# Performance work log

Measured on AMD Instinct MI355X. Metric: run time of the kernel, lower is better.

## Reference

```python
import jax, jax.numpy as jnp
import numpy as np
import math

D = 192            # base channel dim (init arg d); s has D channels
D2 = 2 * D         # y has 2d channels
H = 48; W = 48; BS = 2
NH = 8             # attention heads (divides both D2 and D)
NY = H * W         # tokens per image


def pe2d(d_model, height, width):
    """Faithful port of positionalencoding2d: (d_model, H, W)."""
    dh = d_model // 2
    div = jnp.exp(jnp.arange(0.0, dh, 2.0) * (-math.log(10000.0) / dh))  # (dh/2,)
    pw = jnp.arange(0.0, width)[:, None] * div    # (W, dh/2)
    ph = jnp.arange(0.0, height)[:, None] * div   # (H, dh/2)
    pe = jnp.zeros((d_model, height, width), jnp.float32)
    pe = pe.at[0:dh:2].set(jnp.broadcast_to(jnp.sin(pw).T[:, None, :], (dh // 2, height, width)))
    pe = pe.at[1:dh:2].set(jnp.broadcast_to(jnp.cos(pw).T[:, None, :], (dh // 2, height, width)))
    pe = pe.at[dh::2].set(jnp.broadcast_to(jnp.sin(ph).T[:, :, None], (dh // 2, height, width)))
    pe = pe.at[dh + 1::2].set(jnp.broadcast_to(jnp.cos(ph).T[:, :, None], (dh // 2, height, width)))
    return pe


def conv1x1(x, w, b):
    # x: (b,c,h,w), w: (out,c)
    return jnp.einsum('bchw,oc->bohw', x, w) + b[None, :, None, None]


def conv3x3(x, w, b):
    out = jax.lax.conv_general_dilated(x, w, (1, 1), 'SAME',
                                       dimension_numbers=('NCHW', 'OIHW', 'NCHW'))
    return out + b[None, :, None, None]


def bn(x, g, b):
    # inference-mode batchnorm with zero-mean / unit-var running stats
    return x * g[None, :, None, None] + b[None, :, None, None]


def setup_inputs() -> dict:
    key = jax.random.key(0)
    ks = jax.random.split(key, 8)
    r = lambda k, shp: jax.random.normal(k, shp, jnp.float32) * 0.02
    return {
        'y': jax.random.normal(ks[0], (BS, D2, H, W), jnp.float32),
        's': jax.random.normal(ks[1], (BS, D, H, W), jnp.float32),
        'wq_w': r(ks[2], (D2, D2)), 'wq_b': jnp.zeros((D2,), jnp.float32),
        'wk_w': r(ks[3], (D2, D2)), 'wk_b': jnp.zeros((D2,), jnp.float32),
        'wv_w': r(ks[4], (D, D)),   'wv_b': jnp.zeros((D,), jnp.float32),
        'conv1_w': r(ks[5], (D2, D2)), 'conv1_b': jnp.zeros((D2,), jnp.float32),
        'bn1_g': jnp.ones((D2,), jnp.float32), 'bn1_b': jnp.zeros((D2,), jnp.float32),
        'conv2_w': r(ks[6], (D, D)), 'conv2_b': jnp.zeros((D,), jnp.float32),
        'bn2_g': jnp.ones((D,), jnp.float32), 'bn2_b': jnp.zeros((D,), jnp.float32),
        'up_w': r(ks[7], (D2, D2, 3, 3)), 'up_b': jnp.zeros((D2,), jnp.float32),
        'conv3_w': r(jax.random.fold_in(key, 10), (D, D2)), 'conv3_b': jnp.zeros((D,), jnp.float32),
        'bn3_g': jnp.ones((D,), jnp.float32), 'bn3_b': jnp.zeros((D,), jnp.float32),
        'sig_w': r(jax.random.fold_in(key, 11), (D, D)), 'sig_b': jnp.zeros((D,), jnp.float32),
        'bnsig_g': jnp.ones((D,), jnp.float32), 'bnsig_b': jnp.zeros((D,), jnp.float32),
    }


def reference(y, s, wq_w, wq_b, wk_w, wk_b, wv_w, wv_b,
              conv1_w, conv1_b, bn1_g, bn1_b,
              conv2_w, conv2_b, bn2_g, bn2_b,
              up_w, up_b, conv3_w, conv3_b, bn3_g, bn3_b,
              sig_w, sig_b, bnsig_g, bnsig_b):
    bs = y.shape[0]
    y = y + pe2d(D2, H, W)[None]
    s = s + pe2d(D, H, W)[None]
    # conv+BN+ReLU feature extraction
    y_c1 = jax.nn.relu(bn(conv1x1(y, conv1_w, conv1_b), bn1_g, bn1_b))
    s_c2 = jax.nn.relu(bn(conv1x1(s, conv2_w, conv2_b), bn2_g, bn2_b))
    y_c3 = conv3x3(y, up_w, up_b)                                   # 'up' branch conv
    y_c3 = jax.nn.relu(bn(conv1x1(y_c3, conv3_w, conv3_b), bn3_g, bn3_b))  # (b, D, H, W)
    # tokenize
    yt = y_c1.reshape(bs, D2, NY).transpose(0, 2, 1)   # (b, ny, 2d)
    st = s_c2.reshape(bs, D, NY).transpose(0, 2, 1)    # (b, ny, d)
    # multi-head cross attention: Q,K from y-tokens, V from s-tokens
    Q = (yt @ wq_w.T + wq_b).reshape(bs, NY, NH, D2 // NH).transpose(0, 2, 1, 3)  # (b,h,ny,2d/h)
    K = (yt @ wk_w.T + wk_b).reshape(bs, NY, NH, D2 // NH).transpose(0, 2, 1, 3)
    V = (st @ wv_w.T + wv_b).reshape(bs, NY, NH, D // NH).transpose(0, 2, 1, 3)   # (b,h,ny,d/h)
    M = jnp.einsum('bhnd,bhmd->bhnm', Q, K) / math.sqrt(D)  # scale = d**0.5 as in source
    A = jax.nn.softmax(M, axis=-1)
    Z = jnp.einsum('bhnm,bhmd->bhnd', A, V)                 # (b,h,ny,d/h)
    Z = Z.transpose(0, 2, 1, 3).reshape(bs, NY, D).transpose(0, 2, 1).reshape(bs, D, H, W)
    # sigmoid gate and fuse
    g = jax.nn.sigmoid(bn(conv1x1(Z, sig_w, sig_b), bnsig_g, bnsig_b))
    Z = g * s
    return jnp.concatenate([Z, y_c3], axis=1)               # (b, 2d, H, W)
```

## Files before the change

kernel.cpp:

```cpp
#include <hip/hip_runtime.h>
#include <hip/hip_bf16.h>

#define Dc   192
#define D2c  384
#define NYc  2304

#define QSCALE 0.1041175462f

typedef __attribute__((ext_vector_type(8))) short short8;
typedef __attribute__((ext_vector_type(4))) float f32x4;

__device__ __forceinline__ unsigned short f2bf(float f) {
    unsigned int u = __float_as_uint(f);
    u += 0x7FFFu + ((u >> 16) & 1u);
    return (unsigned short)(u >> 16);
}
__device__ __forceinline__ float fexp2(float x) {
    float r; asm("v_exp_f32 %0, %1" : "=v"(r) : "v"(x)); return r;
}
__device__ __forceinline__ unsigned cvtpk(float lo, float hi) {
    unsigned r; asm("v_cvt_pk_bf16_f32 %0, %1, %2" : "=v"(r) : "v"(lo), "v"(hi));
    return r;
}
__device__ __forceinline__ int swz8(int bid, int nwg) {
    return (bid & 7) * (nwg >> 3) + (bid >> 3);
}

__global__ __launch_bounds__(256)
void build_pe_kernel(float* __restrict__ peY, float* __restrict__ peS) {
    int idx = blockIdx.x * 256 + threadIdx.x;
    int c, p, C; float* dst; int off;
    if (idx < 18432) { c = idx / 48; p = idx % 48; C = 384; dst = peY; off = idx; }
    else { int k = idx - 18432; c = k / 48; p = k % 48; C = 192; dst = peS; off = k; }
    int dh = C >> 1;
    int i = ((c < dh) ? c : c - dh) >> 1;
    float divv = expf((float)(2 * i) * (-9.210340371976184f / (float)dh));
    float ang = (float)p * divv;
    dst[off] = (c & 1) ? cosf(ang) : sinf(ang);
}

__global__ __launch_bounds__(256)
void prep_pe_kernel(const float* __restrict__ y, const float* __restrict__ s,
                    const float* __restrict__ peY, const float* __restrict__ peS,
                    unsigned short* __restrict__ ytok, unsigned short* __restrict__ stok,
                    float* __restrict__ sch) {
    __shared__ unsigned short T[64][66];
    int bid = blockIdx.x;
    int b, ct, nt, C; const float* in; const float* pe; unsigned short* outp; bool isS;
    if (bid < 432) { isS = false; b = bid / 216; int r = bid % 216; ct = r / 36; nt = r % 36;
                     in = y; pe = peY; outp = ytok; C = 384; }
    else { int l = bid - 432; isS = true; b = l / 108; int r = l % 108; ct = r / 36; nt = r % 36;
           in = s; pe = peS; outp = stok; C = 192; }
    int t = threadIdx.x;
    int nl = t & 63;
    int n = nt * 64 + nl;
    int pos_x = n % 48, pos_y = n / 48;
    #pragma unroll
    for (int i = 0; i < 16; ++i) {
        int cl = (t >> 6) + 4 * i;
        int c = ct * 64 + cl;
        int pos = (c < (C >> 1)) ? pos_x : pos_y;
        long gi = (long)b * C * NYc + (long)c * NYc + n;
        float v = in[gi] + pe[c * 48 + pos];
        if (isS) sch[gi] = v;
        T[nl][cl] = f2bf(v);
    }
    __syncthreads();
    #pragma unroll
    for (int i = 0; i < 8; ++i) {
        int nl2 = (t >> 5) + 8 * i;
        int cp  = t & 31;
        unsigned u = (unsigned)T[nl2][2 * cp] | ((unsigned)T[nl2][2 * cp + 1] << 16);
        long row = (long)b * NYc + nt * 64 + nl2;
        *(unsigned*)(outp + row * C + ct * 64 + 2 * cp) = u;
    }
}

__global__ __launch_bounds__(256)
void prep_w_kernel(const float* __restrict__ w0, const float* __restrict__ w1,
                   const float* __restrict__ w2, const float* __restrict__ w3,
                   const float* __restrict__ w4, const float* __restrict__ w5,
                   const float* __restrict__ w6, unsigned short* __restrict__ dst,
                   const float* __restrict__ wq_b, const float* __restrict__ wk_b,
                   float* __restrict__ qkb,
                   const float* __restrict__ upw, unsigned short* __restrict__ upwt) {
    int idx = blockIdx.x * 256 + threadIdx.x;
    if (idx < 626688) {
        if (idx < 768)
            qkb[idx] = (idx < 384) ? wq_b[idx] * QSCALE : wk_b[idx - 384];
        const float* src; int off; float scl = 1.0f;
        if      (idx < 147456) { src = w0; off = idx; }
        else if (idx < 294912) { src = w1; off = idx - 147456; scl = QSCALE; }
        else if (idx < 442368) { src = w2; off = idx - 294912; }
        else if (idx < 479232) { src = w3; off = idx - 442368; }
        else if (idx < 516096) { src = w4; off = idx - 479232; }
        else if (idx < 552960) { src = w5; off = idx - 516096; }
        else                   { src = w6; off = idx - 552960; }
        dst[idx] = f2bf(src[off] * scl);
    } else {
        int k = idx - 626688;
        int o = k / 3456; int r = k % 3456;
        int tap = r / 384;  int c = r % 384;
        upwt[k] = f2bf(upw[((long)o * 384 + c) * 9 + tap]);
    }
}

struct Seg {
    const unsigned short* A; const unsigned short* B;
    int aP, bP, K, nT, blkOff, nBlk, flags;
    const float *bias, *bng, *bnb;
    char* out; int oPitch; long oBatch;
};

template<int NSEG>
__global__ __launch_bounds__(256)
void fused_gemm(Seg s0, Seg s1, Seg s2, const float* __restrict__ smul)
{
    int raw = blockIdx.x;
    Seg sg = s0;
    if (NSEG > 1 && raw >= s1.blkOff) sg = s1;
    if (NSEG > 2 && raw >= s2.blkOff) sg = s2;
    int local = raw - sg.blkOff;
    local = (local & 7) * (sg.nBlk >> 3) + (local >> 3);
    int mt = local / sg.nT, nt = local - mt * sg.nT;
    int m0 = mt * 64, n0 = nt * 64;

    __shared__ __align__(16) unsigned short As[64][72];
    __shared__ __align__(16) unsigned short Bs[64][72];

    int t = threadIdx.x, lane = t & 63, w = t >> 6;
    int lr = lane & 15, lg = lane >> 4;
    int wm = (w >> 1) * 32, wn = (w & 1) * 32;

    f32x4 acc[2][2];
    #pragma unroll
    for (int i = 0; i < 2; ++i)
        #pragma unroll
        for (int j = 0; j < 2; ++j)
            acc[i][j] = (f32x4){0.f, 0.f, 0.f, 0.f};

    uint4 ra[2], rb[2];
    bool im2col = (sg.flags & 1) != 0;

    auto load = [&](int k0) {
        #pragma unroll
        for (int i = 0; i < 2; ++i) {
            int idx = t + i * 256, row = idx >> 3, sl = idx & 7;
            if (im2col) {
                int tok = m0 + row;
                int bb = tok >= NYc;
                int n = tok - bb * NYc;
                int tap = k0 / 384;
                int rem = k0 - tap * 384 + sl * 8;
                int py = n / 48 + tap / 3 - 1;
                int px = n % 48 + tap % 3 - 1;
                ra[i] = (py >= 0 && py < 48 && px >= 0 && px < 48)
                    ? *(const uint4*)(sg.A + ((long)bb * NYc + py * 48 + px) * sg.aP + rem)
                    : make_uint4(0, 0, 0, 0);
            } else {
                ra[i] = *(const uint4*)(sg.A + (long)(m0 + row) * sg.aP + k0 + sl * 8);
            }
            rb[i] = *(const uint4*)(sg.B + (long)(n0 + row) * sg.bP + k0 + sl * 8);
        }
    };
    auto store = [&]() {
        #pragma unroll
        for (int i = 0; i < 2; ++i) {
            int idx = t + i * 256;
            *(uint4*)&As[idx >> 3][(idx & 7) * 8] = ra[i];
            *(uint4*)&Bs[idx >> 3][(idx & 7) * 8] = rb[i];
        }
    };

    load(0); store(); __syncthreads();
    int NT = sg.K >> 6;
    for (int tt = 0; tt < NT; ++tt) {
        if (tt + 1 < NT) load((tt + 1) << 6);
        #pragma unroll
        for (int kk = 0; kk < 2; ++kk) {
            short8 a0 = *(const short8*)&As[wm + lr][kk * 32 + lg * 8];
            short8 a1 = *(const short8*)&As[wm + 16 + lr][kk * 32 + lg * 8];
            short8 b0 = *(const short8*)&Bs[wn + lr][kk * 32 + lg * 8];
            short8 b1 = *(const short8*)&Bs[wn + 16 + lr][kk * 32 + lg * 8];
            acc[0][0] = __builtin_amdgcn_mfma_f32_16x16x32_bf16(a0, b0, acc[0][0], 0, 0, 0);
            acc[0][1] = __builtin_amdgcn_mfma_f32_16x16x32_bf16(a0, b1, acc[0][1], 0, 0, 0);
            acc[1][0] = __builtin_amdgcn_mfma_f32_16x16x32_bf16(a1, b0, acc[1][0], 0, 0, 0);
            acc[1][1] = __builtin_amdgcn_mfma_f32_16x16x32_bf16(a1, b1, acc[1][1], 0, 0, 0);
        }
        __syncthreads();
        if (tt + 1 < NT) { store(); __syncthreads(); }
    }

    #pragma unroll
    for (int i = 0; i < 2; ++i)
    #pragma unroll
    for (int j = 0; j < 2; ++j)
    #pragma unroll
    for (int r = 0; r < 4; ++r) {
        int gm = m0 + wm + i * 16 + lg * 4 + r;
        int gn = n0 + wn + j * 16 + lr;
        int ch = (sg.flags & 8) ? gm : gn;
        float v = acc[i][j][r] + sg.bias[ch];
        if (sg.flags & 2)
            v = fmaxf(fmaf(v, sg.bng[ch], sg.bnb[ch]), 0.f);
        long o; int b = 0, tok = gn;
        if (sg.flags & 8) {
            b = gn >= NYc; tok = gn - b * NYc;
            o = (long)b * sg.oBatch + (long)gm * sg.oPitch + tok;
        } else {
            o = (long)gm * sg.oPitch + gn;
        }
        if (sg.flags & 16) {
            v = fmaf(v, sg.bng[ch], sg.bnb[ch]);
            v = 1.f / (1.f + __expf(-v));
            v *= smul[(long)b * 442368 + (long)gm * NYc + tok];
        }
        if (sg.flags & 4) ((float*)sg.out)[o] = v;
        else              ((unsigned short*)sg.out)[o] = f2bf(v);
    }
}

__global__ __launch_bounds__(512)
void attn_kernel(const unsigned short* __restrict__ QK,
                 const unsigned short* __restrict__ Vc,
                 unsigned short* __restrict__ Zt)
{
    int nid = swz8(blockIdx.x, 576);
    int qb = nid % 36;
    int bh = nid / 36;
    int b = bh >> 3, h = bh & 7;
    const unsigned short* Qg = QK + (long)b * NYc * 768 + h * 48;
    const unsigned short* Kg = Qg + 384;
    const unsigned short* Vg = Vc + ((long)b * Dc + h * 24) * NYc;
    unsigned short*       Z  = Zt + (long)b * NYc * Dc + h * 24;

    __shared__ __align__(16) unsigned short Ks_[128][72];
    __shared__ __align__(16) unsigned short Vs_[32][136];
    __shared__ __align__(16) unsigned int   Ps_[8][16][36];

    int t = threadIdx.x, lane = t & 63, w = t >> 6;
    int lr = lane & 15, lg = lane >> 4;
    int tm = w >> 1, hf = w & 1;
    int q0 = qb * 64;

    short8 z8 = {0, 0, 0, 0, 0, 0, 0, 0};
    const unsigned short* qrow = Qg + (long)(q0 + tm * 16 + lr) * 768;
    short8 bq0 = *(const short8*)(qrow + lg * 8);
    short8 bq1 = (lg < 2) ? *(const short8*)(qrow + 32 + lg * 8) : z8;

    float m_run = -1e30f, l_run = 0.f;
    f32x4 O0 = {0.f, 0.f, 0.f, 0.f}, O1 = {0.f, 0.f, 0.f, 0.f};

    for (int kt = 0; kt < 18; ++kt) {
        long k0 = kt * 128;
        #pragma unroll
        for (int i = 0; i < 2; ++i) {
            int idx = t + i * 512;
            int row = idx >> 3, sl = idx & 7;
            uint4 v = make_uint4(0, 0, 0, 0);
            if (sl < 6) v = *(const uint4*)(Kg + (k0 + row) * 768 + sl * 8);
            *(uint4*)&Ks_[row][sl * 8] = v;
        }
        if (t < 384) {
            int row = t >> 4, sl = t & 15;
            *(uint4*)&Vs_[row][sl * 8] =
                *(const uint4*)(Vg + (long)row * NYc + k0 + sl * 8);
        }
        __syncthreads();

        f32x4 sS[4];
        #pragma unroll
        for (int ks = 0; ks < 4; ++ks) {
            short8 ak0 = *(const short8*)&Ks_[hf * 64 + ks * 16 + lr][lg * 8];
            short8 ak1 = *(const short8*)&Ks_[hf * 64 + ks * 16 + lr][32 + lg * 8];
            f32x4 c = {0.f, 0.f, 0.f, 0.f};
            c = __builtin_amdgcn_mfma_f32_16x16x32_bf16(ak0, bq0, c, 0, 0, 0);
            c = __builtin_amdgcn_mfma_f32_16x16x32_bf16(ak1, bq1, c, 0, 0, 0);
            sS[ks] = c;
        }

        float tmax = -1e30f;
        #pragma unroll
        for (int ks = 0; ks < 4; ++ks)
            #pragma unroll
            for (int r = 0; r < 4; ++r) tmax = fmaxf(tmax, sS[ks][r]);
        tmax = fmaxf(tmax, __shfl_xor(tmax, 16));
        tmax = fmaxf(tmax, __shfl_xor(tmax, 32));

        if (__any(tmax > m_run + 10.f)) {
            float mn = fmaxf(m_run, tmax);
            float al = fexp2(m_run - mn);
            m_run = mn;
            l_run *= al;
            #pragma unroll
            for (int rr = 0; rr < 4; ++rr) {
                float arr = __shfl(al, (lane & 48) | (lg * 4 + rr));
                O0[rr] *= arr; O1[rr] *= arr;
            }
        }

        float psum = 0.f;
        #pragma unroll
        for (int ks = 0; ks < 4; ++ks) {
            float p0 = fexp2(sS[ks][0] - m_run);
            float p1 = fexp2(sS[ks][1] - m_run);
            float p2 = fexp2(sS[ks][2] - m_run);
            float p3 = fexp2(sS[ks][3] - m_run);
            psum += (p0 + p1) + (p2 + p3);
            Ps_[w][lr][8 * ks + 2 * lg]     = cvtpk(p0, p1);
            Ps_[w][lr][8 * ks + 2 * lg + 1] = cvtpk(p2, p3);
        }
        psum += __shfl_xor(psum, 16);
        psum += __shfl_xor(psum, 32);
        l_run += psum;

        short8 ap0 = *(const short8*)&Ps_[w][lr][4 * lg];
        short8 ap1 = *(const short8*)&Ps_[w][lr][16 + 4 * lg];
        short8 bv00 = *(const short8*)&Vs_[lr][hf * 64 + lg * 8];
        short8 bv01 = *(const short8*)&Vs_[lr][hf * 64 + 32 + lg * 8];
        short8 bv10 = *(const short8*)&Vs_[16 + lr][hf * 64 + lg * 8];
        short8 bv11 = *(const short8*)&Vs_[16 + lr][hf * 64 + 32 + lg * 8];
        O0 = __builtin_amdgcn_mfma_f32_16x16x32_bf16(ap0, bv00, O0, 0, 0, 0);
        O0 = __builtin_amdgcn_mfma_f32_16x16x32_bf16(ap1, bv01, O0, 0, 0, 0);
        O1 = __builtin_amdgcn_mfma_f32_16x16x32_bf16(ap0, bv10, O1, 0, 0, 0);
        O1 = __builtin_amdgcn_mfma_f32_16x16x32_bf16(ap1, bv11, O1, 0, 0, 0);
        __syncthreads();
    }

    float* Cf = (float*)&Ps_[0][0][0];
    float* T = Cf + tm * 576;
    if (hf == 1) {
        #pragma unroll
        for (int j = 0; j < 4; ++j) {
            T[lane * 8 + j]     = O0[j];
            T[lane * 8 + 4 + j] = O1[j];
        }
        if (lane < 16) { T[512 + lane] = m_run; T[528 + lane] = l_run; }
    }
    __syncthreads();
    if (hf == 0) {
        float mB = T[512 + lr], lB = T[528 + lr];
        float mS = fmaxf(m_run, mB);
        float aA = fexp2(m_run - mS), aB = fexp2(mB - mS);
        float invl = 1.f / (l_run * aA + lB * aB);
        float fA = aA * invl, fB = aB * invl;
        #pragma unroll
        for (int rr = 0; rr < 4; ++rr) {
            int src = (lane & 48) | (lg * 4 + rr);
            float gA = __shfl(fA, src), gB = __shfl(fB, src);
            int n = q0 + tm * 16 + lg * 4 + rr;
            unsigned short* zr = Z + (long)n * Dc;
            float z0 = O0[rr] * gA + T[lane * 8 + rr] * gB;
            zr[lr] = f2bf(z0);
            if (lr < 8) {
                float z1 = O1[rr] * gA + T[lane * 8 + 4 + rr] * gB;
                zr[16 + lr] = f2bf(z1);
            }
        }
    }
}

extern "C" void kernel_launch(void* const* d_in, const int* in_sizes, int n_in,
                              void* d_out, int out_size, void* d_ws, size_t ws_size,
                              hipStream_t stream) {
    const float* y       = (const float*)d_in[0];
    const float* s       = (const float*)d_in[1];
    const float* wq_w    = (const float*)d_in[2];
    const float* wq_b    = (const float*)d_in[3];
    const float* wk_w    = (const float*)d_in[4];
    const float* wk_b    = (const float*)d_in[5];
    const float* wv_w    = (const float*)d_in[6];
    const float* wv_b    = (const float*)d_in[7];
    const float* conv1_w = (const float*)d_in[8];
    const float* conv1_b = (const float*)d_in[9];
    const float* bn1_g   = (const float*)d_in[10];
    const float* bn1_b   = (const float*)d_in[11];
    const float* conv2_w = (const float*)d_in[12];
    const float* conv2_b = (const float*)d_in[13];
    const float* bn2_g   = (const float*)d_in[14];
    const float* bn2_b   = (const float*)d_in[15];
    const float* up_w    = (const float*)d_in[16];
    const float* up_b    = (const float*)d_in[17];
    const float* conv3_w = (const float*)d_in[18];
    const float* conv3_b = (const float*)d_in[19];
    const float* bn3_g   = (const float*)d_in[20];
    const float* bn3_b   = (const float*)d_in[21];
    const float* sig_w   = (const float*)d_in[22];
    const float* sig_b   = (const float*)d_in[23];
    const float* bnsig_g = (const float*)d_in[24];
    const float* bnsig_b = (const float*)d_in[25];

    unsigned short* wsp   = (unsigned short*)d_ws;
    unsigned short* wcvt  = wsp;
    unsigned short* upwt  = wcvt + 626688;
    unsigned short* y_pe  = upwt + 1327104;
    unsigned short* s_pe  = y_pe + 1769472;
    unsigned short* y_c1  = s_pe + 884736;
    unsigned short* s_c2  = y_c1 + 1769472;
    unsigned short* y_up  = s_c2 + 884736;
    unsigned short* QKtok = y_up + 1769472;
    unsigned short* Vch   = QKtok + 3538944;
    unsigned short* Ztok  = Vch + 884736;
    float*          s_ch  = (float*)(Ztok + 884736);
    float*          qkb   = s_ch + 884736;
    float*          peY   = qkb + 768;
    float*          peS   = peY + 18432;

    const unsigned short* conv1wb = wcvt;
    const unsigned short* wqkb    = wcvt + 147456;
    const unsigned short* conv2wb = wcvt + 442368;
    const unsigned short* wvb     = wcvt + 479232;
    const unsigned short* sigwb   = wcvt + 516096;
    const unsigned short* conv3wb = wcvt + 552960;

    build_pe_kernel<<<108, 256, 0, stream>>>(peY, peS);
    prep_w_kernel<<<7632, 256, 0, stream>>>(conv1_w, wq_w, wk_w, conv2_w,
                                            wv_w, sig_w, conv3_w, wcvt,
                                            wq_b, wk_b, qkb, up_w, upwt);
    prep_pe_kernel<<<648, 256, 0, stream>>>(y, s, peY, peS, y_pe, s_pe, s_ch);

    Seg sz = {};

    {
        Seg a = { y_pe, upwt, D2c, 9 * D2c, 9 * D2c, 6, 0, 432, 1,
                  up_b, nullptr, nullptr, (char*)y_up, D2c, 0 };
        Seg b = { y_pe, conv1wb, D2c, D2c, D2c, 6, 432, 432, 2,
                  conv1_b, bn1_g, bn1_b, (char*)y_c1, D2c, 0 };
        Seg c = { s_pe, conv2wb, Dc, Dc, Dc, 3, 864, 216, 2,
                  conv2_b, bn2_g, bn2_b, (char*)s_c2, Dc, 0 };
        fused_gemm<3><<<1080, 256, 0, stream>>>(a, b, c, nullptr);
    }
    {
        Seg a = { y_c1, wqkb, D2c, D2c, D2c, 12, 0, 864, 0,
                  qkb, nullptr, nullptr, (char*)QKtok, 768, 0 };
        Seg b = { conv3wb, y_up, D2c, D2c, D2c, 72, 864, 216, 2 | 4 | 8,
                  conv3_b, bn3_g, bn3_b,
                  (char*)((float*)d_out + (long)Dc * NYc), NYc, 884736 };
        Seg c = { wvb, s_c2, Dc, Dc, Dc, 72, 1080, 216, 8,
                  wv_b, nullptr, nullptr, (char*)Vch, NYc, 442368 };
        fused_gemm<3><<<1296, 256, 0, stream>>>(a, b, c, nullptr);
    }
    attn_kernel<<<576, 512, 0, stream>>>(QKtok, Vch, Ztok);
    {
        Seg a = { sigwb, Ztok, Dc, Dc, Dc, 72, 0, 216, 4 | 8 | 16,
                  sig_b, bnsig_g, bnsig_b, (char*)d_out, NYc, 884736 };
        fused_gemm<1><<<216, 256, 0, stream>>>(a, sz, sz, s_ch);
    }
}
```

Measured before the change: 198.5 us.

## Fold conv3 into up conv weights, split-K the fused conv, double-buffer GEMM

Since conv3 (1x1) follows the up 3x3 conv with no nonlinearity between them, the change precomposes the conv3 and up weights into one 192x3456 matrix and a combined bias. The fused 3x3-then-1x1 conv then runs as a single split-K (3-way) im2col GEMM whose bf16 partials are summed by a new reduce kernel that applies BN and ReLU. This removes the 384-channel y_up intermediate and the separate conv3 GEMM. The GEMM kernel also gains double-buffered LDS with one barrier per K step and a remainder-aware block swizzle. The risks are extra bf16 rounding of the partials and of the composed weights, plus an extra weight-composition GEMM and reduce launch.

```diff
diff --git a/kernel.cpp b/kernel.cpp
--- a/kernel.cpp
+++ b/kernel.cpp
@@ -15,6 +15,9 @@
     u += 0x7FFFu + ((u >> 16) & 1u);
     return (unsigned short)(u >> 16);
 }
+__device__ __forceinline__ float bf2f(unsigned short u) {
+    return __uint_as_float((unsigned)u << 16);
+}
 __device__ __forceinline__ float fexp2(float x) {
     float r; asm("v_exp_f32 %0, %1" : "=v"(r) : "v"(x)); return r;
 }
@@ -22,8 +25,10 @@
     unsigned r; asm("v_cvt_pk_bf16_f32 %0, %1, %2" : "=v"(r) : "v"(lo), "v"(hi));
     return r;
 }
-__device__ __forceinline__ int swz8(int bid, int nwg) {
-    return (bid & 7) * (nwg >> 3) + (bid >> 3);
+__device__ __forceinline__ int swzb(int orig, int nwg) {
+    int q = nwg >> 3, r = nwg & 7, x = orig & 7;
+    int base = (x < r) ? x * (q + 1) : r * (q + 1) + (x - r) * q;
+    return base + (orig >> 3);
 }
 
 __global__ __launch_bounds__(256)
@@ -83,7 +88,9 @@
                    const float* __restrict__ w6, unsigned short* __restrict__ dst,
                    const float* __restrict__ wq_b, const float* __restrict__ wk_b,
                    float* __restrict__ qkb,
-                   const float* __restrict__ upw, unsigned short* __restrict__ upwt) {
+                   const float* __restrict__ upw, unsigned short* __restrict__ upT,
+                   const float* __restrict__ up_b, const float* __restrict__ conv3_b,
+                   float* __restrict__ c3b) {
     int idx = blockIdx.x * 256 + threadIdx.x;
     if (idx < 626688) {
         if (idx < 768)
@@ -97,17 +104,23 @@
         else if (idx < 552960) { src = w5; off = idx - 516096; }
         else                   { src = w6; off = idx - 552960; }
         dst[idx] = f2bf(src[off] * scl);
-    } else {
+    } else if (idx < 1953792) {
         int k = idx - 626688;
-        int o = k / 3456; int r = k % 3456;
-        int tap = r / 384;  int c = r % 384;
-        upwt[k] = f2bf(upw[((long)o * 384 + c) * 9 + tap]);
+        int j = k / 384, m = k % 384;
+        int tap = j / 384, c = j % 384;
+        upT[k] = f2bf(upw[((long)m * 384 + c) * 9 + tap]);
+    } else if (idx < 1953984) {
+        int o = idx - 1953792;
+        float acc = 0.f;
+        for (int m = 0; m < 384; ++m) acc += w6[o * 384 + m] * up_b[m];
+        c3b[o] = acc + conv3_b[o];
     }
 }
 
 struct Seg {
     const unsigned short* A; const unsigned short* B;
-    int aP, bP, K, nT, blkOff, nBlk, flags;
+    int aP, bP, K, nT, blkOff, nBlk, flags, nSplit;
+    long oSplitBytes;
     const float *bias, *bng, *bnb;
     char* out; int oPitch; long oBatch;
 };
@@ -120,13 +133,20 @@
     Seg sg = s0;
     if (NSEG > 1 && raw >= s1.blkOff) sg = s1;
     if (NSEG > 2 && raw >= s2.blkOff) sg = s2;
-    int local = raw - sg.blkOff;
-    local = (local & 7) * (sg.nBlk >> 3) + (local >> 3);
+    int local = swzb(raw - sg.blkOff, sg.nBlk);
+    int kBase = 0;
+    if (sg.nSplit > 1) {
+        int pc = sg.nBlk / sg.nSplit;
+        int g = local / pc; local -= g * pc;
+        sg.A += (long)g * sg.K;
+        sg.out += (long)g * sg.oSplitBytes;
+        kBase = g * sg.K;
+    }
     int mt = local / sg.nT, nt = local - mt * sg.nT;
     int m0 = mt * 64, n0 = nt * 64;
 
-    __shared__ __align__(16) unsigned short As[64][72];
-    __shared__ __align__(16) unsigned short Bs[64][72];
+    __shared__ __align__(16) unsigned short As[2][64][72];
+    __shared__ __align__(16) unsigned short Bs[2][64][72];
 
     int t = threadIdx.x, lane = t & 63, w = t >> 6;
     int lr = lane & 15, lg = lane >> 4;
@@ -140,55 +160,59 @@
             acc[i][j] = (f32x4){0.f, 0.f, 0.f, 0.f};
 
     uint4 ra[2], rb[2];
-    bool im2col = (sg.flags & 1) != 0;
+    bool im2colB = (sg.flags & 1) != 0;
 
     auto load = [&](int k0) {
         #pragma unroll
         for (int i = 0; i < 2; ++i) {
             int idx = t + i * 256, row = idx >> 3, sl = idx & 7;
-            if (im2col) {
-                int tok = m0 + row;
+            ra[i] = *(const uint4*)(sg.A + (long)(m0 + row) * sg.aP + k0 + sl * 8);
+            if (im2colB) {
+                int tok = n0 + row;
                 int bb = tok >= NYc;
                 int n = tok - bb * NYc;
-                int tap = k0 / 384;
-                int rem = k0 - tap * 384 + sl * 8;
+                int kk = kBase + k0;
+                int tap = kk / 384;
+                int rem = kk - tap * 384 + sl * 8;
                 int py = n / 48 + tap / 3 - 1;
                 int px = n % 48 + tap % 3 - 1;
-                ra[i] = (py >= 0 && py < 48 && px >= 0 && px < 48)
-                    ? *(const uint4*)(sg.A + ((long)bb * NYc + py * 48 + px) * sg.aP + rem)
+                rb[i] = (py >= 0 && py < 48 && px >= 0 && px < 48)
+                    ? *(const uint4*)(sg.B + ((long)bb * NYc + py * 48 + px) * sg.bP + rem)
                     : make_uint4(0, 0, 0, 0);
             } else {
-                ra[i] = *(const uint4*)(sg.A + (long)(m0 + row) * sg.aP + k0 + sl * 8);
+                rb[i] = *(const uint4*)(sg.B + (long)(n0 + row) * sg.bP + k0 + sl * 8);
             }
-            rb[i] = *(const uint4*)(sg.B + (long)(n0 + row) * sg.bP + k0 + sl * 8);
         }
     };
-    auto store = [&]() {
+    auto store = [&](int buf) {
         #pragma unroll
         for (int i = 0; i < 2; ++i) {
             int idx = t + i * 256;
-            *(uint4*)&As[idx >> 3][(idx & 7) * 8] = ra[i];
-            *(uint4*)&Bs[idx >> 3][(idx & 7) * 8] = rb[i];
+            *(uint4*)&As[buf][idx >> 3][(idx & 7) * 8] = ra[i];
+            *(uint4*)&Bs[buf][idx >> 3][(idx & 7) * 8] = rb[i];
         }
     };
 
-    load(0); store(); __syncthreads();
+    load(0); store(0); __syncthreads();
     int NT = sg.K >> 6;
+    int cur = 0;
     for (int tt = 0; tt < NT; ++tt) {
-        if (tt + 1 < NT) load((tt + 1) << 6);
+        bool more = (tt + 1 < NT);
+        if (more) load((tt + 1) << 6);
         #pragma unroll
         for (int kk = 0; kk < 2; ++kk) {
-            short8 a0 = *(const short8*)&As[wm + lr][kk * 32 + lg * 8];
-            short8 a1 = *(const short8*)&As[wm + 16 + lr][kk * 32 + lg * 8];
-            short8 b0 = *(const short8*)&Bs[wn + lr][kk * 32 + lg * 8];
-            short8 b1 = *(const short8*)&Bs[wn + 16 + lr][kk * 32 + lg * 8];
+            short8 a0 = *(const short8*)&As[cur][wm + lr][kk * 32 + lg * 8];
+            short8 a1 = *(const short8*)&As[cur][wm + 16 + lr][kk * 32 + lg * 8];
+            short8 b0 = *(const short8*)&Bs[cur][wn + lr][kk * 32 + lg * 8];
+            short8 b1 = *(const short8*)&Bs[cur][wn + 16 + lr][kk * 32 + lg * 8];
             acc[0][0] = __builtin_amdgcn_mfma_f32_16x16x32_bf16(a0, b0, acc[0][0], 0, 0, 0);
             acc[0][1] = __builtin_amdgcn_mfma_f32_16x16x32_bf16(a0, b1, acc[0][1], 0, 0, 0);
             acc[1][0] = __builtin_amdgcn_mfma_f32_16x16x32_bf16(a1, b0, acc[1][0], 0, 0, 0);
             acc[1][1] = __builtin_amdgcn_mfma_f32_16x16x32_bf16(a1, b1, acc[1][1], 0, 0, 0);
         }
+        if (more) store(cur ^ 1);
         __syncthreads();
-        if (tt + 1 < NT) { store(); __syncthreads(); }
+        cur ^= 1;
     }
 
     #pragma unroll
@@ -200,7 +224,8 @@
         int gm = m0 + wm + i * 16 + lg * 4 + r;
         int gn = n0 + wn + j * 16 + lr;
         int ch = (sg.flags & 8) ? gm : gn;
-        float v = acc[i][j][r] + sg.bias[ch];
+        float v = acc[i][j][r];
+        if (!(sg.flags & 32)) v += sg.bias[ch];
         if (sg.flags & 2)
             v = fmaxf(fmaf(v, sg.bng[ch], sg.bnb[ch]), 0.f);
         long o; int b = 0, tok = gn;
@@ -220,12 +245,38 @@
     }
 }
 
+__global__ __launch_bounds__(256)
+void reduce_up_kernel(const unsigned short* __restrict__ part,
+                      const float* __restrict__ c3b,
+                      const float* __restrict__ bn3g, const float* __restrict__ bn3b,
+                      float* __restrict__ out) {
+    int tid = blockIdx.x * 256 + threadIdx.x;
+    int e = tid * 4;
+    int b = e / 442368; int r = e - b * 442368;
+    int o = r / 2304;
+    ushort4 p0 = *(const ushort4*)(part + e);
+    ushort4 p1 = *(const ushort4*)(part + 884736 + e);
+    ushort4 p2 = *(const ushort4*)(part + 1769472 + e);
+    float g = bn3g[o], bb = bn3b[o], cb = c3b[o];
+    float4 res;
+    float* rp = (float*)&res;
+    unsigned short* q0 = (unsigned short*)&p0;
+    unsigned short* q1 = (unsigned short*)&p1;
+    unsigned short* q2 = (unsigned short*)&p2;
+    #pragma unroll
+    for (int j = 0; j < 4; ++j) {
+        float v = bf2f(q0[j]) + bf2f(q1[j]) + bf2f(q2[j]) + cb;
+        rp[j] = fmaxf(fmaf(v, g, bb), 0.f);
+    }
+    *(float4*)(out + (long)b * 884736 + 442368 + r) = res;
+}
+
 __global__ __launch_bounds__(512)
 void attn_kernel(const unsigned short* __restrict__ QK,
                  const unsigned short* __restrict__ Vc,
                  unsigned short* __restrict__ Zt)
 {
-    int nid = swz8(blockIdx.x, 576);
+    int nid = swzb(blockIdx.x, 576);
     int qb = nid % 36;
     int bh = nid / 36;
     int b = bh >> 3, h = bh & 7;
@@ -392,18 +443,20 @@
 
     unsigned short* wsp   = (unsigned short*)d_ws;
     unsigned short* wcvt  = wsp;
-    unsigned short* upwt  = wcvt + 626688;
-    unsigned short* y_pe  = upwt + 1327104;
+    unsigned short* upT   = wcvt + 626688;
+    unsigned short* Wc    = upT + 1327104;
+    unsigned short* y_pe  = Wc + 663552;
     unsigned short* s_pe  = y_pe + 1769472;
     unsigned short* y_c1  = s_pe + 884736;
     unsigned short* s_c2  = y_c1 + 1769472;
-    unsigned short* y_up  = s_c2 + 884736;
-    unsigned short* QKtok = y_up + 1769472;
+    unsigned short* QKtok = s_c2 + 884736;
     unsigned short* Vch   = QKtok + 3538944;
-    unsigned short* Ztok  = Vch + 884736;
-    float*          s_ch  = (float*)(Ztok + 884736);
+    unsigned short* partZ = Vch + 884736;
+    unsigned short* Ztok  = partZ;
+    float*          s_ch  = (float*)(partZ + 2654208);
     float*          qkb   = s_ch + 884736;
-    float*          peY   = qkb + 768;
+    float*          c3b   = qkb + 768;
+    float*          peY   = c3b + 192;
     float*          peS   = peY + 18432;
 
     const unsigned short* conv1wb = wcvt;
@@ -414,35 +467,41 @@
     const unsigned short* conv3wb = wcvt + 552960;
 
     build_pe_kernel<<<108, 256, 0, stream>>>(peY, peS);
-    prep_w_kernel<<<7632, 256, 0, stream>>>(conv1_w, wq_w, wk_w, conv2_w,
+    prep_w_kernel<<<7633, 256, 0, stream>>>(conv1_w, wq_w, wk_w, conv2_w,
                                             wv_w, sig_w, conv3_w, wcvt,
-                                            wq_b, wk_b, qkb, up_w, upwt);
+                                            wq_b, wk_b, qkb, up_w, upT,
+                                            up_b, conv3_b, c3b);
     prep_pe_kernel<<<648, 256, 0, stream>>>(y, s, peY, peS, y_pe, s_pe, s_ch);
 
     Seg sz = {};
 
     {
-        Seg a = { y_pe, upwt, D2c, 9 * D2c, 9 * D2c, 6, 0, 432, 1,
-                  up_b, nullptr, nullptr, (char*)y_up, D2c, 0 };
-        Seg b = { y_pe, conv1wb, D2c, D2c, D2c, 6, 432, 432, 2,
-                  conv1_b, bn1_g, bn1_b, (char*)y_c1, D2c, 0 };
-        Seg c = { s_pe, conv2wb, Dc, Dc, Dc, 3, 864, 216, 2,
-                  conv2_b, bn2_g, bn2_b, (char*)s_c2, Dc, 0 };
-        fused_gemm<3><<<1080, 256, 0, stream>>>(a, b, c, nullptr);
+        Seg a = { conv3wb, upT, 384, 384, 384, 54, 0, 162, 32, 1, 0,
+                  nullptr, nullptr, nullptr, (char*)Wc, 3456, 0 };
+        fused_gemm<1><<<162, 256, 0, stream>>>(a, sz, sz, nullptr);
     }
     {
-        Seg a = { y_c1, wqkb, D2c, D2c, D2c, 12, 0, 864, 0,
+        Seg a = { Wc, y_pe, 3456, 384, 1152, 72, 0, 648, 1 | 8 | 32, 3,
+                  (long)884736 * 2,
+                  nullptr, nullptr, nullptr, (char*)partZ, NYc, 442368 };
+        Seg b = { y_pe, conv1wb, 384, 384, 384, 6, 648, 432, 2, 1, 0,
+                  conv1_b, bn1_g, bn1_b, (char*)y_c1, 384, 0 };
+        Seg c = { s_pe, conv2wb, 192, 192, 192, 3, 1080, 216, 2, 1, 0,
+                  conv2_b, bn2_g, bn2_b, (char*)s_c2, 192, 0 };
+        fused_gemm<3><<<1296, 256, 0, stream>>>(a, b, c, nullptr);
+    }
+    {
+        Seg a = { y_c1, wqkb, 384, 384, 384, 12, 0, 864, 0, 1, 0,
                   qkb, nullptr, nullptr, (char*)QKtok, 768, 0 };
-        Seg b = { conv3wb, y_up, D2c, D2c, D2c, 72, 864, 216, 2 | 4 | 8,
-                  conv3_b, bn3_g, bn3_b,
-                  (char*)((float*)d_out + (long)Dc * NYc), NYc, 884736 };
-        Seg c = { wvb, s_c2, Dc, Dc, Dc, 72, 1080, 216, 8,
+        Seg b = { wvb, s_c2, 192, 192, 192, 72, 864, 216, 8, 1, 0,
                   wv_b, nullptr, nullptr, (char*)Vch, NYc, 442368 };
-        fused_gemm<3><<<1296, 256, 0, stream>>>(a, b, c, nullptr);
-    }
+        fused_gemm<2><<<1080, 256, 0, stream>>>(a, b, sz, nullptr);
+    }
+    reduce_up_kernel<<<864, 256, 0, stream>>>(partZ, c3b, bn3_g, bn3_b,
+                                              (float*)d_out);
     attn_kernel<<<576, 512, 0, stream>>>(QKtok, Vch, Ztok);
     {
-        Seg a = { sigwb, Ztok, Dc, Dc, Dc, 72, 0, 216, 4 | 8 | 16,
+        Seg a = { sigwb, Ztok, 192, 192, 192, 72, 0, 216, 4 | 8 | 16, 1, 0,
                   sig_b, bnsig_g, bnsig_b, (char*)d_out, NYc, 884736 };
         fused_gemm<1><<<216, 256, 0, stream>>>(a, sz, sz, s_ch);
     }
```

Result: faster. 187.0 us (-5.8%).
